# Optimization experiments

Measured on AMD Instinct MI355X. Metric: run time of the kernel, lower is better.

The kernel has to match this reference:

```python
import jax, jax.numpy as jnp
import numpy as np

B, N, DEPTH = 64, 196, 6
EMBED = 384; CDIM = 384; DIM = EMBED + CDIM            # 768
HEADS = 8; DH = 64; INNER = HEADS * DH                 # 512
VD = INNER + CDIM; DV = VD // HEADS                    # 896, 112
SCALE = DH ** -0.5
EPS = 1e-5


def _bn(x, g, b):
    # BatchNorm1d in training mode applied to (b, e, n): per-channel stats over (b, n)
    m = x.mean(axis=(0, 1))
    v = x.var(axis=(0, 1))  # biased variance, as torch BN uses for normalization
    return (x - m) * jax.lax.rsqrt(v + EPS) * g + b


def setup_inputs() -> dict:
    key = jax.random.key(0)
    ks = jax.random.split(key, 8)
    s = 0.02
    d = {}
    d["x"] = jax.random.normal(ks[0], (B, N, DIM), jnp.float32)
    d["bn1_g"] = jnp.ones((DEPTH, DIM), jnp.float32)
    d["bn1_b"] = jnp.zeros((DEPTH, DIM), jnp.float32)
    d["Wqk"] = jax.random.normal(ks[1], (DEPTH, EMBED, 2 * INNER), jnp.float32) * s
    d["bqk"] = jnp.zeros((DEPTH, 2 * INNER), jnp.float32)
    d["Wv"] = jax.random.normal(ks[2], (DEPTH, DIM, VD), jnp.float32) * s
    d["bv"] = jnp.zeros((DEPTH, VD), jnp.float32)
    d["Wo"] = jax.random.normal(ks[3], (DEPTH, VD, DIM), jnp.float32) * s
    d["bo"] = jnp.zeros((DEPTH, DIM), jnp.float32)
    d["bn2_g"] = jnp.ones((DEPTH, DIM), jnp.float32)
    d["bn2_b"] = jnp.zeros((DEPTH, DIM), jnp.float32)
    d["W1"] = jax.random.normal(ks[4], (DEPTH, DIM, DIM), jnp.float32) * s
    d["b1"] = jnp.zeros((DEPTH, DIM), jnp.float32)
    d["bn3_g"] = jnp.ones((DEPTH, DIM), jnp.float32)
    d["bn3_b"] = jnp.zeros((DEPTH, DIM), jnp.float32)
    d["W2"] = jax.random.normal(ks[5], (DEPTH, DIM, DIM), jnp.float32) * s
    d["b2"] = jnp.zeros((DEPTH, DIM), jnp.float32)
    return d


def reference(x, bn1_g, bn1_b, Wqk, bqk, Wv, bv, Wo, bo,
              bn2_g, bn2_b, W1, b1, bn3_g, bn3_b, W2, b2):
    for i in range(DEPTH):
        # PreNorm(BatchNorm) + Attention + residual
        h = _bn(x, bn1_g[i], bn1_b[i])
        qk = h[:, :, -CDIM:] @ Wqk[i] + bqk[i]          # (B,N,2*INNER) from class slice
        q, k = jnp.split(qk, 2, axis=-1)
        v = h @ Wv[i] + bv[i]                            # (B,N,VD) from full dim
        q = q.reshape(B, N, HEADS, DH).transpose(0, 2, 1, 3)   # b h n d
        k = k.reshape(B, N, HEADS, DH).transpose(0, 2, 1, 3)
        v = v.reshape(B, N, HEADS, DV).transpose(0, 2, 1, 3)
        attn = jax.nn.softmax(jnp.einsum('bhnd,bhmd->bhnm', q, k) * SCALE, axis=-1)
        o = jnp.einsum('bhnm,bhmd->bhnd', attn, v)
        o = o.transpose(0, 2, 1, 3).reshape(B, N, VD)
        x = x + (o @ Wo[i] + bo[i])
        # PreNorm(BatchNorm) + FeedForward (Linear -> BN -> GELU -> Linear) + residual
        h = _bn(x, bn2_g[i], bn2_b[i])
        f = _bn(h @ W1[i] + b1[i], bn3_g[i], bn3_b[i])
        f = jax.nn.gelu(f, approximate=False)            # torch nn.GELU default (exact)
        x = x + (f @ W2[i] + b2[i])
    return x
```

## Files before the change

### kernel.cpp

```cpp
#include <hip/hip_runtime.h>
#include <hip/hip_bf16.h>
#include <stdint.h>


typedef __bf16 bf16x8 __attribute__((ext_vector_type(8)));
typedef __bf16 bf16x4 __attribute__((ext_vector_type(4)));
typedef float  f32x4  __attribute__((ext_vector_type(4)));

#define DIM_  768
#define SCALE_ 0.125f

__device__ __forceinline__ void gload16(const void* g, void* l) {
  __builtin_amdgcn_global_load_lds(
      (__attribute__((address_space(1))) void*)(g),
      (__attribute__((address_space(3))) void*)(l), 16, 0, 0);
}

__global__ void transpose_cvt(const float* __restrict__ W, __bf16* __restrict__ WT,
                              int K, int N) {
  __shared__ float t[32][33];
  const size_t zoff = (size_t)blockIdx.z * K * N;
  W  += zoff; WT += zoff;
  const int bx = blockIdx.x * 32;
  const int by = blockIdx.y * 32;
  for (int j = threadIdx.y; j < 32; j += 8)
    t[j][threadIdx.x] = W[(size_t)(by + j) * N + bx + threadIdx.x];
  __syncthreads();
  for (int j = threadIdx.y; j < 32; j += 8)
    WT[(size_t)(bx + j) * K + by + threadIdx.x] = (__bf16)t[threadIdx.x][j];
}

__global__ void copy_f32(const float* __restrict__ src, float* __restrict__ dst) {
  const int i = blockIdx.x * 256 + threadIdx.x;
  *(f32x4*)(dst + (size_t)i * 4) = *(const f32x4*)(src + (size_t)i * 4);
}

__global__ void bn_stats_part(const float* __restrict__ x, float* __restrict__ part) {
  const int col = blockIdx.x * 256 + threadIdx.x;
  const int r0  = blockIdx.y * 64;
  const float* p = x + (size_t)r0 * DIM_ + col;
  float s = 0.f, s2 = 0.f;
  for (int r = 0; r < 64; ++r) {
    float v = p[(size_t)r * DIM_];
    s += v; s2 += v * v;
  }
  float* q = part + ((size_t)blockIdx.y * DIM_ + col) * 2;
  q[0] = s; q[1] = s2;
}

__global__ void bn_stats_fin(const float* __restrict__ part, const float* __restrict__ g,
                             const float* __restrict__ b, float* __restrict__ sc) {
  const int col = blockIdx.x * 256 + threadIdx.x;
  float s = 0.f, s2 = 0.f;
  for (int p = 0; p < 196; ++p) {
    s  += part[((size_t)p * DIM_ + col) * 2];
    s2 += part[((size_t)p * DIM_ + col) * 2 + 1];
  }
  const float mean = s * (1.f / 12544.f);
  const float var  = s2 * (1.f / 12544.f) - mean * mean;
  const float rstd = rsqrtf(var + 1e-5f);
  const float scale = rstd * g[col];
  sc[col]        = scale;
  sc[DIM_ + col] = b[col] - mean * scale;
}

__global__ void bn_fin2(float* __restrict__ acc, const float* __restrict__ g,
                        const float* __restrict__ b, float* __restrict__ sc) {
  const int col = blockIdx.x * 256 + threadIdx.x;
  const float s  = acc[col * 2];
  const float s2 = acc[col * 2 + 1];
  acc[col * 2] = 0.f; acc[col * 2 + 1] = 0.f;
  const float mean = s * (1.f / 12544.f);
  const float var  = s2 * (1.f / 12544.f) - mean * mean;
  const float rstd = rsqrtf(var + 1e-5f);
  const float scale = rstd * g[col];
  sc[col]        = scale;
  sc[DIM_ + col] = b[col] - mean * scale;
}

__global__ void bn_apply_f32(const float* __restrict__ x, const float* __restrict__ sc,
                             __bf16* __restrict__ h) {
  const int i = blockIdx.x * 256 + threadIdx.x;
  const int c4 = i % 192;
  f32x4 v  = *(const f32x4*)(x + (size_t)i * 4);
  f32x4 scl = *(const f32x4*)(sc + c4 * 4);
  f32x4 sh  = *(const f32x4*)(sc + DIM_ + c4 * 4);
  f32x4 y = v * scl + sh;
  bf16x4 o;
  o[0] = (__bf16)y[0]; o[1] = (__bf16)y[1]; o[2] = (__bf16)y[2]; o[3] = (__bf16)y[3];
  *(bf16x4*)(h + (size_t)i * 4) = o;
}

__global__ void bn_gelu_apply(const __bf16* __restrict__ f1, const float* __restrict__ sc,
                              __bf16* __restrict__ h) {
  const int i = blockIdx.x * 256 + threadIdx.x;
  const int c4 = i % 192;
  bf16x4 v4 = *(const bf16x4*)(f1 + (size_t)i * 4);
  f32x4 scl = *(const f32x4*)(sc + c4 * 4);
  f32x4 sh  = *(const f32x4*)(sc + DIM_ + c4 * 4);
  bf16x4 o;
#pragma unroll
  for (int j = 0; j < 4; ++j) {
    float y = (float)v4[j] * scl[j] + sh[j];
    float gl = 0.5f * y * (1.f + erff(y * 0.70710678118654752f));
    o[j] = (__bf16)gl;
  }
  *(bf16x4*)(h + (size_t)i * 4) = o;
}

template <int EPI, int STATS, int PANEL_X>
__global__ __launch_bounds__(256, 2) void gemm128(
    const __bf16* __restrict__ A, int lda,
    const __bf16* __restrict__ BT, int K,
    const float* __restrict__ bias,
    __bf16* __restrict__ outB, float* outF, int ldc,
    float* __restrict__ statsAcc, int P, int S) {
  __shared__ __bf16 sA[128 * 64];
  __shared__ __bf16 sB[128 * 64];
  const int bid = blockIdx.x;
  const int xcd = bid & 7, r0b = bid >> 3;
  const int pl = r0b / S, sh = r0b - pl * S;
  const int p = pl * 8 + xcd;
  if (p >= P) return;
  const int mx = PANEL_X ? p : sh;
  const int ny = PANEL_X ? sh : p;

  const int tid = threadIdx.x;
  const int lane = tid & 63, wv = tid >> 6;
  const int l15 = lane & 15, hi = lane >> 4;
  const int m0 = mx * 128, n0 = ny * 128;
  const __bf16* Ab = A + (size_t)m0 * lda;
  const __bf16* Bb = BT + (size_t)n0 * K;
  const int wr = (wv >> 1) * 64, wc = (wv & 1) * 64;

  f32x4 acc[4][4] = {};

#define STAGE(kt)                                                             \
  {                                                                           \
    const int k0_ = (kt) << 6;                                                \
    _Pragma("unroll")                                                         \
    for (int i_ = 0; i_ < 4; ++i_) {                                          \
      const int o_ = i_ * 4096 + tid * 16;                                    \
      const int row_ = o_ >> 7;                                               \
      const int j_ = (o_ >> 4) & 7;                                           \
      const int src_ = (j_ ^ (row_ & 7)) << 3;                                \
      gload16(Ab + (size_t)row_ * lda + k0_ + src_,                           \
              &sA[i_ * 2048 + wv * 512]);                                     \
      gload16(Bb + (size_t)row_ * K + k0_ + src_,                             \
              &sB[i_ * 2048 + wv * 512]);                                     \
    }                                                                         \
  }

  const int nkt = K >> 6;
  for (int kt = 0; kt < nkt; ++kt) {
    if (kt) __syncthreads();
    STAGE(kt);
    asm volatile("s_waitcnt vmcnt(0)" ::: "memory");
    __syncthreads();
    const char* cA = (const char*)sA;
    const char* cB = (const char*)sB;
#pragma unroll
    for (int ks = 0; ks < 2; ++ks) {
      bf16x8 af[4], bfr[4];
#pragma unroll
      for (int m = 0; m < 4; ++m) {
        const int row = wr + m * 16 + l15;
        af[m] = *(const bf16x8*)(cA + row * 128 +
                                 ((ks * 64 + hi * 16) ^ ((row & 7) << 4)));
      }
#pragma unroll
      for (int n = 0; n < 4; ++n) {
        const int row = wc + n * 16 + l15;
        bfr[n] = *(const bf16x8*)(cB + row * 128 +
                                  ((ks * 64 + hi * 16) ^ ((row & 7) << 4)));
      }
#pragma unroll
      for (int m = 0; m < 4; ++m)
#pragma unroll
        for (int n = 0; n < 4; ++n)
          acc[m][n] = __builtin_amdgcn_mfma_f32_16x16x32_bf16(af[m], bfr[n], acc[m][n], 0, 0, 0);
    }
  }
#undef STAGE

  float* scol = (float*)sA;
  if (STATS) {
    __syncthreads();
    scol[tid] = 0.f;
    __syncthreads();
  }

  float cs[4], cs2[4];
  if (STATS)
#pragma unroll
    for (int n = 0; n < 4; ++n) { cs[n] = 0.f; cs2[n] = 0.f; }

#pragma unroll
  for (int m = 0; m < 4; ++m)
#pragma unroll
    for (int n = 0; n < 4; ++n) {
      const int cc = n0 + wc + n * 16 + l15;
      const float bc = (EPI == 2) ? 0.f : bias[cc];
#pragma unroll
      for (int r = 0; r < 4; ++r) {
        const int rr = m0 + wr + m * 16 + hi * 4 + r;
        const float val = acc[m][n][r] + ((EPI == 2) ? bias[rr] : bc);
        float fv;
        if (EPI == 1) {
          float* pp = outF + (size_t)rr * ldc + cc;
          fv = *pp + val;
          *pp = fv;
        } else {
          fv = val;
          outB[(size_t)rr * ldc + cc] = (__bf16)fv;
        }
        if (STATS) { cs[n] += fv; cs2[n] += fv * fv; }
      }
    }

  if (STATS) {
#pragma unroll
    for (int n = 0; n < 4; ++n) {
      float s = cs[n], s2 = cs2[n];
      s += __shfl_xor(s, 16); s2 += __shfl_xor(s2, 16);
      s += __shfl_xor(s, 32); s2 += __shfl_xor(s2, 32);
      if (lane < 16) {
        atomicAdd(&scol[(wc + n * 16 + l15) * 2], s);
        atomicAdd(&scol[(wc + n * 16 + l15) * 2 + 1], s2);
      }
    }
    __syncthreads();
    if (tid < 128) {
      atomicAdd(&statsAcc[(size_t)(n0 + tid) * 2], scol[tid * 2]);
      atomicAdd(&statsAcc[(size_t)(n0 + tid) * 2 + 1], scol[tid * 2 + 1]);
    }
  }
}

#define SV_OFF 26624
#define SP_OFF 83968
__global__ __launch_bounds__(512, 1) void attn_kernel(
    const __bf16* __restrict__ qk, const __bf16* __restrict__ vT,
    __bf16* __restrict__ og) {
  __shared__ __align__(16) char smem[149504];
  const int bh = blockIdx.x, bb = bh >> 3, hh = bh & 7;
  const int tid = threadIdx.x, lane = tid & 63, wv = tid >> 6;
  const int l15 = lane & 15, hi = lane >> 4;

  const __bf16* qbase = qk + (size_t)bb * (196 * 1024) + hh * 64;
  const __bf16* kbase = qbase + 512;
  const __bf16* vbase = vT + (size_t)(hh * 112) * 12544 + bb * 196;
  __bf16* obase = og + (size_t)bb * (196 * 896) + hh * 112;

  char* sV = smem + SV_OFF;
  char* sP = smem + SP_OFF + wv * 8192;

  for (int s = tid; s < 1664; s += 512) {
    const int n = s >> 3, j = s & 7;
    const int row = (n < 196) ? n : 195;
    const int k8 = j ^ (n & 7);
    gload16(kbase + (size_t)row * 1024 + k8 * 8, smem + ((s >> 6) << 10));
  }
  for (int c = tid; c < 112 * 49; c += 512) {
    const int d = c / 49, c8 = c - d * 49;
    const bf16x4 v4 = *(const bf16x4*)(vbase + (size_t)d * 12544 + c8 * 4);
    *(bf16x4*)(sV + d * 512 + ((c8 * 8) ^ ((d & 7) << 4))) = v4;
  }
  {
    bf16x4 z = {};
    for (int c = tid; c < 112 * 7; c += 512) {
      const int d = c / 7, c8 = 49 + (c - d * 7);
      *(bf16x4*)(sV + d * 512 + ((c8 * 8) ^ ((d & 7) << 4))) = z;
    }
  }
  asm volatile("s_waitcnt vmcnt(0)" ::: "memory");
  __syncthreads();

  const int xm = (l15 & 7) << 4;
  for (int qt = wv; qt < 13; qt += 8) {
    const int q0 = qt * 16;
    int qn = q0 + l15; if (qn > 195) qn = 195;
    const __bf16* qp = qbase + (size_t)qn * 1024 + hi * 8;
    const bf16x8 qa0 = *(const bf16x8*)(qp);
    const bf16x8 qa1 = *(const bf16x8*)(qp + 32);

    f32x4 s[13] = {};
#pragma unroll
    for (int nf = 0; nf < 13; ++nf) {
      const int j = nf * 16 + l15;
      const bf16x8 kb0 = *(const bf16x8*)(smem + j * 128 + ((hi * 16) ^ xm));
      const bf16x8 kb1 = *(const bf16x8*)(smem + j * 128 + ((64 + hi * 16) ^ xm));
      s[nf] = __builtin_amdgcn_mfma_f32_16x16x32_bf16(qa0, kb0, s[nf], 0, 0, 0);
      s[nf] = __builtin_amdgcn_mfma_f32_16x16x32_bf16(qa1, kb1, s[nf], 0, 0, 0);
    }

#pragma unroll
    for (int r = 0; r < 4; ++r) {
      float mx = -3.0e38f;
#pragma unroll
      for (int nf = 0; nf < 12; ++nf) mx = fmaxf(mx, s[nf][r]);
      if (l15 < 4) mx = fmaxf(mx, s[12][r]);
#pragma unroll
      for (int off = 1; off < 16; off <<= 1) mx = fmaxf(mx, __shfl_xor(mx, off));
      float sum = 0.f;
#pragma unroll
      for (int nf = 0; nf < 13; ++nf) {
        const bool valid = (nf < 12) || (l15 < 4);
        const float p = valid ? __expf((s[nf][r] - mx) * SCALE_) : 0.f;
        s[nf][r] = p; sum += p;
      }
#pragma unroll
      for (int off = 1; off < 16; off <<= 1) sum += __shfl_xor(sum, off);
      const float inv = 1.f / sum;
#pragma unroll
      for (int nf = 0; nf < 13; ++nf) s[nf][r] *= inv;
    }

#pragma unroll
    for (int r = 0; r < 4; ++r) {
      const int row = hi * 4 + r;
      const int rm = (row & 7) << 4;
      char* rp = sP + row * 512;
#pragma unroll
      for (int nf = 0; nf < 13; ++nf)
        *(__bf16*)(rp + (((nf * 16 + l15) * 2) ^ rm)) = (__bf16)s[nf][r];
      *(__bf16*)(rp + (((208 + l15) * 2) ^ rm)) = (__bf16)0.f;
    }

    f32x4 oa[7] = {};
#pragma unroll
    for (int kk = 0; kk < 7; ++kk) {
      const bf16x8 pa = *(const bf16x8*)(sP + l15 * 512 + ((kk * 64 + hi * 16) ^ xm));
#pragma unroll
      for (int nf = 0; nf < 7; ++nf) {
        const int d = nf * 16 + l15;
        const bf16x8 vbf = *(const bf16x8*)(sV + d * 512 + ((kk * 64 + hi * 16) ^ xm));
        oa[nf] = __builtin_amdgcn_mfma_f32_16x16x32_bf16(pa, vbf, oa[nf], 0, 0, 0);
      }
    }
#pragma unroll
    for (int nf = 0; nf < 7; ++nf)
#pragma unroll
      for (int r = 0; r < 4; ++r) {
        const int q = q0 + hi * 4 + r;
        if (q < 196) obase[(size_t)q * 896 + nf * 16 + l15] = (__bf16)oa[nf][r];
      }
  }
}

extern "C" void kernel_launch(void* const* d_in, const int* in_sizes, int n_in,
                              void* d_out, int out_size, void* d_ws, size_t ws_size,
                              hipStream_t stream) {
  (void)in_sizes; (void)n_in; (void)out_size; (void)ws_size;
  const float* x_in  = (const float*)d_in[0];
  const float* bn1_g = (const float*)d_in[1];
  const float* bn1_b = (const float*)d_in[2];
  const float* Wqk   = (const float*)d_in[3];
  const float* bqk   = (const float*)d_in[4];
  const float* Wv    = (const float*)d_in[5];
  const float* bv    = (const float*)d_in[6];
  const float* Wo    = (const float*)d_in[7];
  const float* bo    = (const float*)d_in[8];
  const float* bn2_g = (const float*)d_in[9];
  const float* bn2_b = (const float*)d_in[10];
  const float* W1    = (const float*)d_in[11];
  const float* b1    = (const float*)d_in[12];
  const float* bn3_g = (const float*)d_in[13];
  const float* bn3_b = (const float*)d_in[14];
  const float* W2    = (const float*)d_in[15];
  const float* b2    = (const float*)d_in[16];

  char* ws = (char*)d_ws;
  float*  xb   = (float*)(ws + 0);
  __bf16* wqkT = (__bf16*)(ws + 38535168);
  __bf16* wvT  = (__bf16*)(ws + 43253760);
  __bf16* woT  = (__bf16*)(ws + 51511296);
  __bf16* w1T  = (__bf16*)(ws + 59768832);
  __bf16* w2T  = (__bf16*)(ws + 66846720);
  __bf16* hb   = (__bf16*)(ws + 73924608);
  __bf16* qkb  = (__bf16*)(ws + 93192192);
  __bf16* vTb  = (__bf16*)(ws + 118882304);
  __bf16* obuf = (__bf16*)(ws + 141361152);
  float*  part = (float*)(ws + 163840000);
  float*  sc   = (float*)(ws + 165044224);
  float*  sAcc = (float*)(ws + 165051392);
  __bf16* f1b  = qkb;

  const dim3 tb(256);

  transpose_cvt<<<dim3(32, 12, 6), dim3(32, 8), 0, stream>>>(Wqk, wqkT, 384, 1024);
  transpose_cvt<<<dim3(28, 24, 6), dim3(32, 8), 0, stream>>>(Wv,  wvT,  768, 896);
  transpose_cvt<<<dim3(24, 28, 6), dim3(32, 8), 0, stream>>>(Wo,  woT,  896, 768);
  transpose_cvt<<<dim3(24, 24, 6), dim3(32, 8), 0, stream>>>(W1,  w1T,  768, 768);
  transpose_cvt<<<dim3(24, 24, 6), dim3(32, 8), 0, stream>>>(W2,  w2T,  768, 768);
  copy_f32<<<9408, tb, 0, stream>>>(x_in, xb);
  hipMemsetAsync(sAcc, 0, 768 * 2 * sizeof(float), stream);

  bn_stats_part<<<dim3(3, 196), tb, 0, stream>>>(xb, part);
  bn_stats_fin<<<3, tb, 0, stream>>>(part, bn1_g, bn1_b, sc);

  const int gQK = 8 * 13 * 8;
  const int gV  = 8 * 13 * 7;
  const int gO  = 8 * 13 * 6;

  for (int i = 0; i < 6; ++i) {
    const __bf16* wqkT_i = wqkT + (size_t)i * 1024 * 384;
    const __bf16* wvT_i  = wvT  + (size_t)i * 896 * 768;
    const __bf16* woT_i  = woT  + (size_t)i * 768 * 896;
    const __bf16* w1T_i  = w1T  + (size_t)i * 768 * 768;
    const __bf16* w2T_i  = w2T  + (size_t)i * 768 * 768;

    bn_apply_f32<<<9408, tb, 0, stream>>>(xb, sc, hb);
    gemm128<0, 0, 1><<<gQK, tb, 0, stream>>>(hb + 384, 768, wqkT_i, 384,
                                             bqk + i * 1024, qkb, nullptr, 1024,
                                             nullptr, 98, 8);
    gemm128<2, 0, 0><<<gV, tb, 0, stream>>>(wvT_i, 768, hb, 768,
                                            bv + i * 896, vTb, nullptr, 12544,
                                            nullptr, 98, 7);
    attn_kernel<<<512, dim3(512), 0, stream>>>(qkb, vTb, obuf);
    gemm128<1, 1, 1><<<gO, tb, 0, stream>>>(obuf, 896, woT_i, 896,
                                            bo + i * 768, nullptr, xb, 768,
                                            sAcc, 98, 6);

    bn_fin2<<<3, tb, 0, stream>>>(sAcc, bn2_g + i * 768, bn2_b + i * 768, sc);
    bn_apply_f32<<<9408, tb, 0, stream>>>(xb, sc, hb);
    gemm128<0, 1, 1><<<gO, tb, 0, stream>>>(hb, 768, w1T_i, 768,
                                            b1 + i * 768, f1b, nullptr, 768,
                                            sAcc, 98, 6);
    bn_fin2<<<3, tb, 0, stream>>>(sAcc, bn3_g + i * 768, bn3_b + i * 768, sc);
    bn_gelu_apply<<<9408, tb, 0, stream>>>(f1b, sc, hb);
    if (i < 5) {
      gemm128<1, 1, 1><<<gO, tb, 0, stream>>>(hb, 768, w2T_i, 768,
                                              b2 + i * 768, nullptr, xb, 768,
                                              sAcc, 98, 6);
      bn_fin2<<<3, tb, 0, stream>>>(sAcc, bn1_g + (i + 1) * 768, bn1_b + (i + 1) * 768, sc);
    } else {
      gemm128<1, 0, 1><<<gO, tb, 0, stream>>>(hb, 768, w2T_i, 768,
                                              b2 + i * 768, nullptr, xb, 768,
                                              nullptr, 98, 6);
    }
  }
  copy_f32<<<9408, tb, 0, stream>>>(xb, (float*)d_out);
}
```

Measured before the change: 1.408 ms.

## Shrink GEMM tiles to 64x128 and keep attention probabilities in registers

The GEMM tile changes from 128x128 to 64x128 and the launch grids double, so more blocks fill the GPU and occupancy rises (launch bounds go from 2 to 6 blocks per SM). The attention kernel computes S transposed, packs the probabilities to bf16 with v_cvt_pk_bf16 and moves them into the PV operand layout with cross-lane shuffles, so the LDS staging of P is gone. It also shrinks the V padding and LDS footprint so four blocks can share a CU, and reorganises the softmax reduction. In exchange the GEMMs do more A/B reloads per output, and the attention kernel adds shuffle overhead.

```diff
diff --git a/kernel.cpp b/kernel.cpp
--- a/kernel.cpp
+++ b/kernel.cpp
@@ -14,6 +14,12 @@
   __builtin_amdgcn_global_load_lds(
       (__attribute__((address_space(1))) void*)(g),
       (__attribute__((address_space(3))) void*)(l), 16, 0, 0);
+}
+
+__device__ __forceinline__ uint32_t cvt_pk_bf16(float lo, float hi) {
+  uint32_t r;
+  asm("v_cvt_pk_bf16_f32 %0, %1, %2" : "=v"(r) : "v"(lo), "v"(hi));
+  return r;
 }
 
 __global__ void transpose_cvt(const float* __restrict__ W, __bf16* __restrict__ WT,
@@ -109,13 +115,13 @@
 }
 
 template <int EPI, int STATS, int PANEL_X>
-__global__ __launch_bounds__(256, 2) void gemm128(
+__global__ __launch_bounds__(256, 6) void gemm64(
     const __bf16* __restrict__ A, int lda,
     const __bf16* __restrict__ BT, int K,
     const float* __restrict__ bias,
     __bf16* __restrict__ outB, float* outF, int ldc,
     float* __restrict__ statsAcc, int P, int S) {
-  __shared__ __bf16 sA[128 * 64];
+  __shared__ __bf16 sA[64 * 64];
   __shared__ __bf16 sB[128 * 64];
   const int bid = blockIdx.x;
   const int xcd = bid & 7, r0b = bid >> 3;
@@ -128,42 +134,42 @@
   const int tid = threadIdx.x;
   const int lane = tid & 63, wv = tid >> 6;
   const int l15 = lane & 15, hi = lane >> 4;
-  const int m0 = mx * 128, n0 = ny * 128;
+  const int m0 = mx * 64, n0 = ny * 128;
   const __bf16* Ab = A + (size_t)m0 * lda;
   const __bf16* Bb = BT + (size_t)n0 * K;
-  const int wr = (wv >> 1) * 64, wc = (wv & 1) * 64;
-
-  f32x4 acc[4][4] = {};
-
-#define STAGE(kt)                                                             \
-  {                                                                           \
-    const int k0_ = (kt) << 6;                                                \
-    _Pragma("unroll")                                                         \
-    for (int i_ = 0; i_ < 4; ++i_) {                                          \
-      const int o_ = i_ * 4096 + tid * 16;                                    \
-      const int row_ = o_ >> 7;                                               \
-      const int j_ = (o_ >> 4) & 7;                                           \
-      const int src_ = (j_ ^ (row_ & 7)) << 3;                                \
-      gload16(Ab + (size_t)row_ * lda + k0_ + src_,                           \
-              &sA[i_ * 2048 + wv * 512]);                                     \
-      gload16(Bb + (size_t)row_ * K + k0_ + src_,                             \
-              &sB[i_ * 2048 + wv * 512]);                                     \
-    }                                                                         \
-  }
+  const int wr = (wv >> 1) * 32, wc = (wv & 1) * 64;
+
+  f32x4 acc[2][4] = {};
 
   const int nkt = K >> 6;
   for (int kt = 0; kt < nkt; ++kt) {
     if (kt) __syncthreads();
-    STAGE(kt);
+    const int k0 = kt << 6;
+#pragma unroll
+    for (int i_ = 0; i_ < 2; ++i_) {
+      const int o = i_ * 4096 + tid * 16;
+      const int row = o >> 7;
+      const int j = (o >> 4) & 7;
+      const int src = (j ^ (row & 7)) << 3;
+      gload16(Ab + (size_t)row * lda + k0 + src, &sA[i_ * 2048 + wv * 512]);
+    }
+#pragma unroll
+    for (int i_ = 0; i_ < 4; ++i_) {
+      const int o = i_ * 4096 + tid * 16;
+      const int row = o >> 7;
+      const int j = (o >> 4) & 7;
+      const int src = (j ^ (row & 7)) << 3;
+      gload16(Bb + (size_t)row * K + k0 + src, &sB[i_ * 2048 + wv * 512]);
+    }
     asm volatile("s_waitcnt vmcnt(0)" ::: "memory");
     __syncthreads();
     const char* cA = (const char*)sA;
     const char* cB = (const char*)sB;
 #pragma unroll
     for (int ks = 0; ks < 2; ++ks) {
-      bf16x8 af[4], bfr[4];
-#pragma unroll
-      for (int m = 0; m < 4; ++m) {
+      bf16x8 af[2], bfr[4];
+#pragma unroll
+      for (int m = 0; m < 2; ++m) {
         const int row = wr + m * 16 + l15;
         af[m] = *(const bf16x8*)(cA + row * 128 +
                                  ((ks * 64 + hi * 16) ^ ((row & 7) << 4)));
@@ -175,13 +181,12 @@
                                   ((ks * 64 + hi * 16) ^ ((row & 7) << 4)));
       }
 #pragma unroll
-      for (int m = 0; m < 4; ++m)
+      for (int m = 0; m < 2; ++m)
 #pragma unroll
         for (int n = 0; n < 4; ++n)
           acc[m][n] = __builtin_amdgcn_mfma_f32_16x16x32_bf16(af[m], bfr[n], acc[m][n], 0, 0, 0);
     }
   }
-#undef STAGE
 
   float* scol = (float*)sA;
   if (STATS) {
@@ -196,7 +201,7 @@
     for (int n = 0; n < 4; ++n) { cs[n] = 0.f; cs2[n] = 0.f; }
 
 #pragma unroll
-  for (int m = 0; m < 4; ++m)
+  for (int m = 0; m < 2; ++m)
 #pragma unroll
     for (int n = 0; n < 4; ++n) {
       const int cc = n0 + wc + n * 16 + l15;
@@ -237,14 +242,14 @@
   }
 }
 
-#define SV_OFF 26624
-#define SP_OFF 83968
-__global__ __launch_bounds__(512, 1) void attn_kernel(
+#define SVOFF 25088
+__global__ __launch_bounds__(512, 4) void attn_kernel(
     const __bf16* __restrict__ qk, const __bf16* __restrict__ vT,
     __bf16* __restrict__ og) {
-  __shared__ __align__(16) char smem[149504];
+  __shared__ __align__(16) char smem[75264];
   const int bh = blockIdx.x, bb = bh >> 3, hh = bh & 7;
-  const int tid = threadIdx.x, lane = tid & 63, wv = tid >> 6;
+  const int tid = threadIdx.x, lane = tid & 63;
+  const int wv = tid >> 6;
   const int l15 = lane & 15, hi = lane >> 4;
 
   const __bf16* qbase = qk + (size_t)bb * (196 * 1024) + hh * 64;
@@ -252,31 +257,22 @@
   const __bf16* vbase = vT + (size_t)(hh * 112) * 12544 + bb * 196;
   __bf16* obase = og + (size_t)bb * (196 * 896) + hh * 112;
 
-  char* sV = smem + SV_OFF;
-  char* sP = smem + SP_OFF + wv * 8192;
-
-  for (int s = tid; s < 1664; s += 512) {
+  char* sV = smem + SVOFF;
+
+  for (int s = tid; s < 1568; s += 512) {
     const int n = s >> 3, j = s & 7;
-    const int row = (n < 196) ? n : 195;
     const int k8 = j ^ (n & 7);
-    gload16(kbase + (size_t)row * 1024 + k8 * 8, smem + ((s >> 6) << 10));
-  }
-  for (int c = tid; c < 112 * 49; c += 512) {
-    const int d = c / 49, c8 = c - d * 49;
-    const bf16x4 v4 = *(const bf16x4*)(vbase + (size_t)d * 12544 + c8 * 4);
-    *(bf16x4*)(sV + d * 512 + ((c8 * 8) ^ ((d & 7) << 4))) = v4;
-  }
-  {
-    bf16x4 z = {};
-    for (int c = tid; c < 112 * 7; c += 512) {
-      const int d = c / 7, c8 = 49 + (c - d * 7);
-      *(bf16x4*)(sV + d * 512 + ((c8 * 8) ^ ((d & 7) << 4))) = z;
-    }
+    gload16(kbase + (size_t)n * 1024 + k8 * 8, smem + ((s >> 6) << 10));
+  }
+  for (int c = tid; c < 112 * 56; c += 512) {
+    const int d = c / 56, c8 = c - d * 56;
+    bf16x4 v4 = {};
+    if (c8 < 49) v4 = *(const bf16x4*)(vbase + (size_t)d * 12544 + c8 * 4);
+    *(bf16x4*)(sV + d * 448 + ((c8 * 8) ^ ((d & 3) << 4))) = v4;
   }
   asm volatile("s_waitcnt vmcnt(0)" ::: "memory");
   __syncthreads();
 
-  const int xm = (l15 & 7) << 4;
   for (int qt = wv; qt < 13; qt += 8) {
     const int q0 = qt * 16;
     int qn = q0 + l15; if (qn > 195) qn = 195;
@@ -287,55 +283,79 @@
     f32x4 s[13] = {};
 #pragma unroll
     for (int nf = 0; nf < 13; ++nf) {
-      const int j = nf * 16 + l15;
-      const bf16x8 kb0 = *(const bf16x8*)(smem + j * 128 + ((hi * 16) ^ xm));
-      const bf16x8 kb1 = *(const bf16x8*)(smem + j * 128 + ((64 + hi * 16) ^ xm));
-      s[nf] = __builtin_amdgcn_mfma_f32_16x16x32_bf16(qa0, kb0, s[nf], 0, 0, 0);
-      s[nf] = __builtin_amdgcn_mfma_f32_16x16x32_bf16(qa1, kb1, s[nf], 0, 0, 0);
-    }
-
+      int j = nf * 16 + l15; if (j > 195) j = 195;
+      const int sw = (j & 7) << 4;
+      const bf16x8 kb0 = *(const bf16x8*)(smem + j * 128 + ((hi * 16) ^ sw));
+      const bf16x8 kb1 = *(const bf16x8*)(smem + j * 128 + ((64 + hi * 16) ^ sw));
+      s[nf] = __builtin_amdgcn_mfma_f32_16x16x32_bf16(kb0, qa0, s[nf], 0, 0, 0);
+      s[nf] = __builtin_amdgcn_mfma_f32_16x16x32_bf16(kb1, qa1, s[nf], 0, 0, 0);
+    }
+
+    float mx = -3.0e38f;
+#pragma unroll
+    for (int nf = 0; nf < 12; ++nf)
+#pragma unroll
+      for (int r = 0; r < 4; ++r) mx = fmaxf(mx, s[nf][r]);
+    if (hi == 0)
+#pragma unroll
+      for (int r = 0; r < 4; ++r) mx = fmaxf(mx, s[12][r]);
+    mx = fmaxf(mx, __shfl_xor(mx, 16));
+    mx = fmaxf(mx, __shfl_xor(mx, 32));
+    float sum = 0.f;
+#pragma unroll
+    for (int nf = 0; nf < 12; ++nf)
+#pragma unroll
+      for (int r = 0; r < 4; ++r) {
+        const float pv = __expf((s[nf][r] - mx) * SCALE_);
+        s[nf][r] = pv; sum += pv;
+      }
 #pragma unroll
     for (int r = 0; r < 4; ++r) {
-      float mx = -3.0e38f;
-#pragma unroll
-      for (int nf = 0; nf < 12; ++nf) mx = fmaxf(mx, s[nf][r]);
-      if (l15 < 4) mx = fmaxf(mx, s[12][r]);
-#pragma unroll
-      for (int off = 1; off < 16; off <<= 1) mx = fmaxf(mx, __shfl_xor(mx, off));
-      float sum = 0.f;
-#pragma unroll
-      for (int nf = 0; nf < 13; ++nf) {
-        const bool valid = (nf < 12) || (l15 < 4);
-        const float p = valid ? __expf((s[nf][r] - mx) * SCALE_) : 0.f;
-        s[nf][r] = p; sum += p;
-      }
-#pragma unroll
-      for (int off = 1; off < 16; off <<= 1) sum += __shfl_xor(sum, off);
-      const float inv = 1.f / sum;
-#pragma unroll
-      for (int nf = 0; nf < 13; ++nf) s[nf][r] *= inv;
-    }
-
-#pragma unroll
-    for (int r = 0; r < 4; ++r) {
-      const int row = hi * 4 + r;
-      const int rm = (row & 7) << 4;
-      char* rp = sP + row * 512;
-#pragma unroll
-      for (int nf = 0; nf < 13; ++nf)
-        *(__bf16*)(rp + (((nf * 16 + l15) * 2) ^ rm)) = (__bf16)s[nf][r];
-      *(__bf16*)(rp + (((208 + l15) * 2) ^ rm)) = (__bf16)0.f;
-    }
+      const float pv = (hi == 0) ? __expf((s[12][r] - mx) * SCALE_) : 0.f;
+      s[12][r] = pv; sum += pv;
+    }
+    sum += __shfl_xor(sum, 16);
+    sum += __shfl_xor(sum, 32);
+    const float inv = 1.f / sum;
+#pragma unroll
+    for (int nf = 0; nf < 13; ++nf)
+#pragma unroll
+      for (int r = 0; r < 4; ++r) s[nf][r] *= inv;
 
     f32x4 oa[7] = {};
+    const int sLo = l15 + ((hi & 1) << 5);
+    const int sHi = sLo + 16;
+    const bool up = (hi >> 1) != 0;
 #pragma unroll
     for (int kk = 0; kk < 7; ++kk) {
-      const bf16x8 pa = *(const bf16x8*)(sP + l15 * 512 + ((kk * 64 + hi * 16) ^ xm));
+      const uint32_t a0 = cvt_pk_bf16(s[2 * kk][0], s[2 * kk][1]);
+      const uint32_t a1 = cvt_pk_bf16(s[2 * kk][2], s[2 * kk][3]);
+      const uint32_t w0a = (uint32_t)__shfl((int)a0, sLo, 64);
+      const uint32_t w1a = (uint32_t)__shfl((int)a1, sLo, 64);
+      const uint32_t w2a = (uint32_t)__shfl((int)a0, sHi, 64);
+      const uint32_t w3a = (uint32_t)__shfl((int)a1, sHi, 64);
+      uint32_t w0, w1, w2, w3;
+      if (kk < 6) {
+        const uint32_t b0 = cvt_pk_bf16(s[2 * kk + 1][0], s[2 * kk + 1][1]);
+        const uint32_t b1 = cvt_pk_bf16(s[2 * kk + 1][2], s[2 * kk + 1][3]);
+        const uint32_t w0b = (uint32_t)__shfl((int)b0, sLo, 64);
+        const uint32_t w1b = (uint32_t)__shfl((int)b1, sLo, 64);
+        const uint32_t w2b = (uint32_t)__shfl((int)b0, sHi, 64);
+        const uint32_t w3b = (uint32_t)__shfl((int)b1, sHi, 64);
+        w0 = up ? w0b : w0a; w1 = up ? w1b : w1a;
+        w2 = up ? w2b : w2a; w3 = up ? w3b : w3a;
+      } else {
+        w0 = up ? 0u : w0a; w1 = up ? 0u : w1a;
+        w2 = up ? 0u : w2a; w3 = up ? 0u : w3a;
+      }
+      union { uint32_t u[4]; bf16x8 v; } pa;
+      pa.u[0] = w0; pa.u[1] = w1; pa.u[2] = w2; pa.u[3] = w3;
 #pragma unroll
       for (int nf = 0; nf < 7; ++nf) {
         const int d = nf * 16 + l15;
-        const bf16x8 vbf = *(const bf16x8*)(sV + d * 512 + ((kk * 64 + hi * 16) ^ xm));
-        oa[nf] = __builtin_amdgcn_mfma_f32_16x16x32_bf16(pa, vbf, oa[nf], 0, 0, 0);
+        const bf16x8 vbf = *(const bf16x8*)(sV + d * 448 +
+                              ((kk * 64 + hi * 16) ^ ((d & 3) << 4)));
+        oa[nf] = __builtin_amdgcn_mfma_f32_16x16x32_bf16(pa.v, vbf, oa[nf], 0, 0, 0);
       }
     }
 #pragma unroll
@@ -399,9 +419,9 @@
   bn_stats_part<<<dim3(3, 196), tb, 0, stream>>>(xb, part);
   bn_stats_fin<<<3, tb, 0, stream>>>(part, bn1_g, bn1_b, sc);
 
-  const int gQK = 8 * 13 * 8;
-  const int gV  = 8 * 13 * 7;
-  const int gO  = 8 * 13 * 6;
+  const int gQK = 8 * 25 * 8;
+  const int gV  = 8 * 13 * 14;
+  const int gO  = 8 * 25 * 6;
 
   for (int i = 0; i < 6; ++i) {
     const __bf16* wqkT_i = wqkT + (size_t)i * 1024 * 384;
@@ -411,33 +431,33 @@
     const __bf16* w2T_i  = w2T  + (size_t)i * 768 * 768;
 
     bn_apply_f32<<<9408, tb, 0, stream>>>(xb, sc, hb);
-    gemm128<0, 0, 1><<<gQK, tb, 0, stream>>>(hb + 384, 768, wqkT_i, 384,
-                                             bqk + i * 1024, qkb, nullptr, 1024,
-                                             nullptr, 98, 8);
-    gemm128<2, 0, 0><<<gV, tb, 0, stream>>>(wvT_i, 768, hb, 768,
-                                            bv + i * 896, vTb, nullptr, 12544,
-                                            nullptr, 98, 7);
+    gemm64<0, 0, 1><<<gQK, tb, 0, stream>>>(hb + 384, 768, wqkT_i, 384,
+                                            bqk + i * 1024, qkb, nullptr, 1024,
+                                            nullptr, 196, 8);
+    gemm64<2, 0, 0><<<gV, tb, 0, stream>>>(wvT_i, 768, hb, 768,
+                                           bv + i * 896, vTb, nullptr, 12544,
+                                           nullptr, 98, 14);
     attn_kernel<<<512, dim3(512), 0, stream>>>(qkb, vTb, obuf);
-    gemm128<1, 1, 1><<<gO, tb, 0, stream>>>(obuf, 896, woT_i, 896,
-                                            bo + i * 768, nullptr, xb, 768,
-                                            sAcc, 98, 6);
+    gemm64<1, 1, 1><<<gO, tb, 0, stream>>>(obuf, 896, woT_i, 896,
+                                           bo + i * 768, nullptr, xb, 768,
+                                           sAcc, 196, 6);
 
     bn_fin2<<<3, tb, 0, stream>>>(sAcc, bn2_g + i * 768, bn2_b + i * 768, sc);
     bn_apply_f32<<<9408, tb, 0, stream>>>(xb, sc, hb);
-    gemm128<0, 1, 1><<<gO, tb, 0, stream>>>(hb, 768, w1T_i, 768,
-                                            b1 + i * 768, f1b, nullptr, 768,
-                                            sAcc, 98, 6);
+    gemm64<0, 1, 1><<<gO, tb, 0, stream>>>(hb, 768, w1T_i, 768,
+                                           b1 + i * 768, f1b, nullptr, 768,
+                                           sAcc, 196, 6);
     bn_fin2<<<3, tb, 0, stream>>>(sAcc, bn3_g + i * 768, bn3_b + i * 768, sc);
     bn_gelu_apply<<<9408, tb, 0, stream>>>(f1b, sc, hb);
     if (i < 5) {
-      gemm128<1, 1, 1><<<gO, tb, 0, stream>>>(hb, 768, w2T_i, 768,
-                                              b2 + i * 768, nullptr, xb, 768,
-                                              sAcc, 98, 6);
+      gemm64<1, 1, 1><<<gO, tb, 0, stream>>>(hb, 768, w2T_i, 768,
+                                             b2 + i * 768, nullptr, xb, 768,
+                                             sAcc, 196, 6);
       bn_fin2<<<3, tb, 0, stream>>>(sAcc, bn1_g + (i + 1) * 768, bn1_b + (i + 1) * 768, sc);
     } else {
-      gemm128<1, 0, 1><<<gO, tb, 0, stream>>>(hb, 768, w2T_i, 768,
-                                              b2 + i * 768, nullptr, xb, 768,
-                                              nullptr, 98, 6);
+      gemm64<1, 0, 1><<<gO, tb, 0, stream>>>(hb, 768, w2T_i, 768,
+                                             b2 + i * 768, nullptr, xb, 768,
+                                             nullptr, 196, 6);
     }
   }
   copy_f32<<<9408, tb, 0, stream>>>(xb, (float*)d_out);
```

New measurement: 1.758 ms. 24.8% more time.
